# Performance work log

Measured on AMD Instinct MI355X. Metric: run time of the kernel, lower is better.

## Reference

```python
import jax, jax.numpy as jnp
import numpy as np

B, S, D, A = 4, 4096, 1024, 1024

def setup_inputs() -> dict:
    key = jax.random.key(0)
    k1, k2, k3, k4 = jax.random.split(key, 4)
    # weights scaled like keras 'random_normal' init (stddev=0.05)
    return {
        "inputs": jax.random.normal(k1, (B, S, D), dtype=jnp.float32),
        "W_q": jax.random.normal(k2, (D, A), dtype=jnp.float32) * 0.05,
        "W_k": jax.random.normal(k3, (D, A), dtype=jnp.float32) * 0.05,
        "W_v": jax.random.normal(k4, (D, A), dtype=jnp.float32) * 0.05,
    }

def reference(inputs, W_q, W_k, W_v):
    Q = jnp.einsum('bsd,da->bsa', inputs, W_q)
    K = jnp.einsum('bsd,da->bsa', inputs, W_k)
    V = jnp.einsum('bsd,da->bsa', inputs, W_v)
    # NOTE: original layer applies NO 1/sqrt(d) scaling
    scores = jnp.einsum('bqa,bka->bqk', Q, K)            # [B, S, S]
    weights = jax.nn.softmax(scores, axis=-1)
    return jnp.einsum('bqk,bka->bqa', weights, V)        # [B, S, A]
```

## Files before the change

### kernel.cpp

```cpp
#include <hip/hip_runtime.h>
#include <math.h>

constexpr int CS = 4096;
constexpr int CD = 1024;
constexpr int CA = 1024;
constexpr int CB_ = 4;

typedef unsigned short u16;
typedef __bf16 bf16x8 __attribute__((ext_vector_type(8)));
typedef float f32x4 __attribute__((ext_vector_type(4)));
typedef unsigned short u16x4 __attribute__((ext_vector_type(4)));

__device__ __forceinline__ u16 f32_to_bf16(float f) {
  unsigned u = __float_as_uint(f);
  u = (u + 0x7FFF + ((u >> 16) & 1)) >> 16;
  return (u16)u;
}
__device__ __forceinline__ float bf16_to_f32(u16 h) {
  return __uint_as_float(((unsigned)h) << 16);
}

__device__ __forceinline__ void async16(const u16* g, u16* lds_uniform) {
  __builtin_amdgcn_global_load_lds(
      (const __attribute__((address_space(1))) void*)g,
      (__attribute__((address_space(3))) void*)lds_uniform, 16, 0, 0);
}

#define ST_A256(BUF, AP, HALF)                                       \
  do {                                                               \
    const u16* _p = (AP) + roA + ((HALF) ? 128L * lda : 0L);         \
    u16* _d = &lds[(BUF)*32768 + (2 + (HALF)) * 8192 + si0 * 512];   \
    async16(_p, _d);                                                 \
    async16(_p + 32, _d + 512);                                      \
  } while (0)
#define ST_B256(BUF, BP, HALF)                                       \
  do {                                                               \
    const u16* _p = (BP) + roB + ((HALF) ? 128L * ldb : 0L);         \
    u16* _d = &lds[(BUF)*32768 + (HALF)*8192 + si0 * 512];           \
    async16(_p, _d);                                                 \
    async16(_p + 32, _d + 512);                                      \
  } while (0)

#define KITER256(T, DO_S1, DO_S2, VMW)                                        \
  do {                                                                        \
    const int buf = (T)&1;                                                    \
    const int bo_a = buf * 32768 + (2 + wr) * 8192;                           \
    const int bo_b = buf * 32768 + (wc >> 1) * 8192;                          \
    bf16x8 Bf[4][2], Am[2][2], A47[4][2];                                     \
                     \
    _Pragma("unroll") for (int n = 0; n < 4; ++n) _Pragma("unroll")           \
        for (int kk = 0; kk < 2; ++kk) Bf[n][kk] =                            \
        *(const bf16x8*)&lds[bo_b + ((nbase + n) * 2 + kk) * 512 + foff];     \
    _Pragma("unroll") for (int m = 0; m < 2; ++m) _Pragma("unroll")           \
        for (int kk = 0; kk < 2; ++kk) Am[m][kk] =                            \
        *(const bf16x8*)&lds[bo_a + (m * 2 + kk) * 512 + foff];               \
    if (DO_S1) ST_A256(buf ^ 1, a1p, 1);                                      \
    __builtin_amdgcn_s_barrier();                                             \
    asm volatile("s_waitcnt lgkmcnt(0)" ::: "memory");                        \
    __builtin_amdgcn_s_setprio(1);                                            \
    _Pragma("unroll") for (int m = 0; m < 2; ++m) _Pragma("unroll")           \
        for (int n = 0; n < 4; ++n) _Pragma("unroll")                         \
        for (int kk = 0; kk < 2; ++kk) acc[m][n] =                            \
        __builtin_amdgcn_mfma_f32_16x16x32_bf16(Am[m][kk], Bf[n][kk],         \
                                                acc[m][n], 0, 0, 0);          \
    __builtin_amdgcn_s_setprio(0);                                            \
    __builtin_amdgcn_s_barrier();                                             \
                             \
    _Pragma("unroll") for (int m = 0; m < 2; ++m) _Pragma("unroll")           \
        for (int kk = 0; kk < 2; ++kk) Am[m][kk] =                            \
        *(const bf16x8*)&lds[bo_a + ((2 + m) * 2 + kk) * 512 + foff];         \
    if (DO_S2) ST_B256(buf, b2p, 0);                                          \
    __builtin_amdgcn_s_barrier();                                             \
    asm volatile("s_waitcnt lgkmcnt(0)" ::: "memory");                        \
    __builtin_amdgcn_s_setprio(1);                                            \
    _Pragma("unroll") for (int m = 0; m < 2; ++m) _Pragma("unroll")           \
        for (int n = 0; n < 4; ++n) _Pragma("unroll")                         \
        for (int kk = 0; kk < 2; ++kk) acc[2 + m][n] =                        \
        __builtin_amdgcn_mfma_f32_16x16x32_bf16(Am[m][kk], Bf[n][kk],         \
                                                acc[2 + m][n], 0, 0, 0);      \
    __builtin_amdgcn_s_setprio(0);                                            \
    __builtin_amdgcn_s_barrier();                                             \
                             \
    _Pragma("unroll") for (int m = 0; m < 4; ++m) _Pragma("unroll")           \
        for (int kk = 0; kk < 2; ++kk) A47[m][kk] =                           \
        *(const bf16x8*)&lds[bo_a + ((4 + m) * 2 + kk) * 512 + foff];         \
    if (DO_S2) ST_B256(buf, b2p, 1);                                          \
    __builtin_amdgcn_s_barrier();                                             \
    asm volatile("s_waitcnt lgkmcnt(0)" ::: "memory");                        \
    __builtin_amdgcn_s_setprio(1);                                            \
    _Pragma("unroll") for (int m = 0; m < 2; ++m) _Pragma("unroll")           \
        for (int n = 0; n < 4; ++n) _Pragma("unroll")                         \
        for (int kk = 0; kk < 2; ++kk) acc[4 + m][n] =                        \
        __builtin_amdgcn_mfma_f32_16x16x32_bf16(A47[m][kk], Bf[n][kk],        \
                                                acc[4 + m][n], 0, 0, 0);      \
    __builtin_amdgcn_s_setprio(0);                                            \
    __builtin_amdgcn_s_barrier();                                             \
           \
    if (DO_S2) ST_A256(buf, a2p, 0);                                          \
    __builtin_amdgcn_s_barrier();                                             \
    asm volatile("s_waitcnt lgkmcnt(0)" ::: "memory");                        \
    __builtin_amdgcn_s_setprio(1);                                            \
    _Pragma("unroll") for (int m = 0; m < 2; ++m) _Pragma("unroll")           \
        for (int n = 0; n < 4; ++n) _Pragma("unroll")                         \
        for (int kk = 0; kk < 2; ++kk) acc[6 + m][n] =                        \
        __builtin_amdgcn_mfma_f32_16x16x32_bf16(A47[2 + m][kk], Bf[n][kk],    \
                                                acc[6 + m][n], 0, 0, 0);      \
    __builtin_amdgcn_s_setprio(0);                                            \
    VMW;                                                                      \
    __builtin_amdgcn_s_barrier();                                             \
  } while (0)

template <int NSEG>
__global__ __launch_bounds__(512, 2) void gemm256_nt(
    const u16* __restrict__ A0s, const u16* __restrict__ A1s,
    const u16* __restrict__ A2s, const u16* __restrict__ B0s,
    const u16* __restrict__ B1s, const u16* __restrict__ B2s,
    float* __restrict__ C, int Kd, int lda, int ldb, int ldc) {
  __shared__ u16 lds[65536];
  const int tid = threadIdx.x;
  const int wave = tid >> 6, lane = tid & 63;
  const int wr = wave >> 2, wc = wave & 3;
  const int l16 = lane & 15, quad = lane >> 4;
  const int m0 = blockIdx.y * 256, n0 = blockIdx.x * 256;
  const int foff = (l16 * 32 + quad * 8) ^ ((l16 & 8) << 1);
  const int si0 = wave * 2;
  const int srow = lane >> 2;
  const int scol = ((lane & 3) * 8) ^ ((lane & 32) ? 16 : 0);
  const long roA = (long)(m0 + wave * 16 + srow) * lda + scol;
  const long roB = (long)(n0 + wave * 16 + srow) * ldb + scol;
  const int nbase = (wc & 1) * 4;

  f32x4 acc[8][4];
#pragma unroll
  for (int i = 0; i < 8; ++i)
#pragma unroll
    for (int j = 0; j < 4; ++j) acc[i][j] = (f32x4){0.f, 0.f, 0.f, 0.f};

  const int ktps = Kd >> 6;
  const int NT = NSEG * ktps;

  int s1 = 0, k1 = 64;
  if (k1 == Kd) { k1 = 0; s1 = 1; }
  const u16* a1p = (s1 == 0 ? A0s : A1s) + k1;
  const u16* b1p = (s1 == 0 ? B0s : B1s) + k1;
  ST_B256(0, B0s, 0);
  ST_B256(0, B0s, 1);
  ST_A256(0, A0s, 0);
  ST_A256(0, A0s, 1);
  ST_B256(1, b1p, 0);
  ST_B256(1, b1p, 1);
  ST_A256(1, a1p, 0);
  (void)b1p;
  int s2 = s1, k2 = k1 + 64;
  if (k2 == Kd) { k2 = 0; ++s2; }
  const u16* a2p = (s2 == 0 ? A0s : (s2 == 1 ? A1s : A2s)) + k2;
  const u16* b2p = (s2 == 0 ? B0s : (s2 == 1 ? B1s : B2s)) + k2;
  asm volatile("s_waitcnt vmcnt(6)" ::: "memory");
  __builtin_amdgcn_s_barrier();

  for (int t = 0; t + 2 < NT; ++t) {
    KITER256(t, 1, 1, asm volatile("s_waitcnt vmcnt(6)" ::: "memory"));
    a1p = a2p;
    k2 += 64;
    if (k2 == Kd) {
      k2 = 0;
      ++s2;
      a2p = (s2 == 1 ? A1s : A2s);
      b2p = (s2 == 1 ? B1s : B2s);
    } else {
      a2p += 64;
      b2p += 64;
    }
  }
  KITER256(NT - 2, 1, 0, asm volatile("s_waitcnt vmcnt(0)" ::: "memory"));
  KITER256(NT - 1, 0, 0, ((void)0));

  const int rb0 = m0 + wr * 128 + quad * 4;
  const int cc0 = n0 + wc * 64 + l16;
#pragma unroll
  for (int m = 0; m < 8; ++m)
#pragma unroll
    for (int n = 0; n < 4; ++n) {
      const long rb = rb0 + m * 16;
      const int c = cc0 + n * 16;
#pragma unroll
      for (int r = 0; r < 4; ++r) C[(rb + r) * (long)ldc + c] = acc[m][n][r];
    }
}

__global__ __launch_bounds__(512, 2) void gemm256_qk(
    const u16* __restrict__ Xhi, const u16* __restrict__ Xlo,
    const u16* __restrict__ Whi, const u16* __restrict__ Wlo,
    u16* __restrict__ Qhi, u16* __restrict__ Qlo, u16* __restrict__ Khi,
    u16* __restrict__ Klo) {
  __shared__ u16 lds[65536];
  const int tid = threadIdx.x;
  const int wave = tid >> 6, lane = tid & 63;
  const int wr = wave >> 2, wc = wave & 3;
  const int l16 = lane & 15, quad = lane >> 4;
  const int m0 = blockIdx.y * 256, n0 = blockIdx.x * 256;
  const int region = n0 >> 10;
  const int lda = CD, ldb = CD;
  const int foff = (l16 * 32 + quad * 8) ^ ((l16 & 8) << 1);
  const int si0 = wave * 2;
  const int srow = lane >> 2;
  const int scol = ((lane & 3) * 8) ^ ((lane & 32) ? 16 : 0);
  const long roA = (long)(m0 + wave * 16 + srow) * lda + scol;
  const long roB = (long)(n0 + wave * 16 + srow) * ldb + scol;
  const int nbase = (wc & 1) * 4;

  f32x4 acc[8][4];
#pragma unroll
  for (int i = 0; i < 8; ++i)
#pragma unroll
    for (int j = 0; j < 4; ++j) acc[i][j] = (f32x4){0.f, 0.f, 0.f, 0.f};

  const u16* Asegs[3] = {Xhi, Xlo, Xhi};
  const u16* Bsegs[3] = {Whi, Whi, Wlo};
  const int NT = 48;

  const u16* a1p = Xhi + 64;
  int s2 = 0, k2 = 128;
  const u16* a2p = Xhi + 128;
  const u16* b2p = Whi + 128;
  ST_B256(0, Whi, 0);
  ST_B256(0, Whi, 1);
  ST_A256(0, Xhi, 0);
  ST_A256(0, Xhi, 1);
  ST_B256(1, Whi + 64, 0);
  ST_B256(1, Whi + 64, 1);
  ST_A256(1, Xhi + 64, 0);
  asm volatile("s_waitcnt vmcnt(6)" ::: "memory");
  __builtin_amdgcn_s_barrier();

  for (int t = 0; t + 2 < NT; ++t) {
    KITER256(t, 1, 1, asm volatile("s_waitcnt vmcnt(6)" ::: "memory"));
    a1p = a2p;
    k2 += 64;
    if (k2 == CD) {
      k2 = 0;
      ++s2;
      if (s2 < 3) {
        a2p = Asegs[s2];
        b2p = Bsegs[s2];
      }
    } else {
      a2p += 64;
      b2p += 64;
    }
  }
  KITER256(NT - 2, 1, 0, asm volatile("s_waitcnt vmcnt(0)" ::: "memory"));
  KITER256(NT - 1, 0, 0, ((void)0));

  const int rb0 = m0 + wr * 128 + quad * 4;
  const int ccl = (n0 & 1023) + wc * 64 + l16;
  u16* Chi = region ? Khi : Qhi;
  u16* Clo = region ? Klo : Qlo;
#pragma unroll
  for (int m = 0; m < 8; ++m)
#pragma unroll
    for (int n = 0; n < 4; ++n) {
      const long rb = rb0 + m * 16;
      const int c = ccl + n * 16;
#pragma unroll
      for (int r = 0; r < 4; ++r) {
        const float v = acc[m][n][r];
        const u16 h = f32_to_bf16(v);
        Chi[(rb + r) * (long)CA + c] = h;
        Clo[(rb + r) * (long)CA + c] = f32_to_bf16(v - bf16_to_f32(h));
      }
    }
}

__global__ __launch_bounds__(512, 2) void gemm256_v(
    const u16* __restrict__ Xhi, const u16* __restrict__ Wvhi,
    u16* __restrict__ Vt) {
  __shared__ u16 lds[65536];
  const int tid = threadIdx.x;
  const int wave = tid >> 6, lane = tid & 63;
  const int wr = wave >> 2, wc = wave & 3;
  const int l16 = lane & 15, quad = lane >> 4;
  const int m0 = blockIdx.y * 256, n0 = blockIdx.x * 256;
  const int lda = CD, ldb = CD;
  const int foff = (l16 * 32 + quad * 8) ^ ((l16 & 8) << 1);
  const int si0 = wave * 2;
  const int srow = lane >> 2;
  const int scol = ((lane & 3) * 8) ^ ((lane & 32) ? 16 : 0);
  const long roA = (long)(m0 + wave * 16 + srow) * lda + scol;
  const long roB = (long)(n0 + wave * 16 + srow) * ldb + scol;
  const int nbase = (wc & 1) * 4;

  f32x4 acc[8][4];
#pragma unroll
  for (int i = 0; i < 8; ++i)
#pragma unroll
    for (int j = 0; j < 4; ++j) acc[i][j] = (f32x4){0.f, 0.f, 0.f, 0.f};

  const int NT = 16;
  const u16* a1p = Xhi + 64;
  const u16* a2p = Xhi + 128;
  const u16* b2p = Wvhi + 128;
  ST_B256(0, Wvhi, 0);
  ST_B256(0, Wvhi, 1);
  ST_A256(0, Xhi, 0);
  ST_A256(0, Xhi, 1);
  ST_B256(1, Wvhi + 64, 0);
  ST_B256(1, Wvhi + 64, 1);
  ST_A256(1, Xhi + 64, 0);
  asm volatile("s_waitcnt vmcnt(6)" ::: "memory");
  __builtin_amdgcn_s_barrier();

  for (int t = 0; t + 2 < NT; ++t) {
    KITER256(t, 1, 1, asm volatile("s_waitcnt vmcnt(6)" ::: "memory"));
    a1p = a2p;
    a2p += 64;
    b2p += 64;
  }
  KITER256(NT - 2, 1, 0, asm volatile("s_waitcnt vmcnt(0)" ::: "memory"));
  KITER256(NT - 1, 0, 0, ((void)0));

  const int rb0 = m0 + wr * 128 + quad * 4;
  const int ccl = n0 + wc * 64 + l16;
#pragma unroll
  for (int m = 0; m < 8; ++m) {
    const int rg = rb0 + m * 16;
    const long vb = (long)(rg >> 12) * CA * CS;
    const int s = rg & 4095;
#pragma unroll
    for (int n = 0; n < 4; ++n) {
      const int c = ccl + n * 16;
      u16x4 p;
#pragma unroll
      for (int r = 0; r < 4; ++r) p[r] = f32_to_bf16(acc[m][n][r]);
      *(u16x4*)&Vt[vb + (long)c * CS + s] = p;
    }
  }
}

__global__ __launch_bounds__(512, 2) void gemm256_pv(
    const u16* __restrict__ P, const u16* __restrict__ Vtb,
    float* __restrict__ Cp) {
  __shared__ u16 lds[65536];
  const int tid = threadIdx.x;
  const int wave = tid >> 6, lane = tid & 63;
  const int wr = wave >> 2, wc = wave & 3;
  const int l16 = lane & 15, quad = lane >> 4;
  const int m0 = blockIdx.y * 256, n0 = blockIdx.x * 256;
  const int z = blockIdx.z;
  const int lda = CS, ldb = CS;
  const int foff = (l16 * 32 + quad * 8) ^ ((l16 & 8) << 1);
  const int si0 = wave * 2;
  const int srow = lane >> 2;
  const int scol = ((lane & 3) * 8) ^ ((lane & 32) ? 16 : 0);
  const long roA = (long)(m0 + wave * 16 + srow) * lda + scol;
  const long roB = (long)(n0 + wave * 16 + srow) * ldb + scol;
  const int nbase = (wc & 1) * 4;

  f32x4 acc[8][4];
#pragma unroll
  for (int i = 0; i < 8; ++i)
#pragma unroll
    for (int j = 0; j < 4; ++j) acc[i][j] = (f32x4){0.f, 0.f, 0.f, 0.f};

  const u16* A0 = P + (long)z * 1024;
  const u16* B0 = Vtb + (long)z * 1024;
  const int NT = 16;
  const u16* a1p = A0 + 64;
  const u16* a2p = A0 + 128;
  const u16* b2p = B0 + 128;
  ST_B256(0, B0, 0);
  ST_B256(0, B0, 1);
  ST_A256(0, A0, 0);
  ST_A256(0, A0, 1);
  ST_B256(1, B0 + 64, 0);
  ST_B256(1, B0 + 64, 1);
  ST_A256(1, A0 + 64, 0);
  asm volatile("s_waitcnt vmcnt(6)" ::: "memory");
  __builtin_amdgcn_s_barrier();

  for (int t = 0; t + 2 < NT; ++t) {
    KITER256(t, 1, 1, asm volatile("s_waitcnt vmcnt(6)" ::: "memory"));
    a1p = a2p;
    a2p += 64;
    b2p += 64;
  }
  KITER256(NT - 2, 1, 0, asm volatile("s_waitcnt vmcnt(0)" ::: "memory"));
  KITER256(NT - 1, 0, 0, ((void)0));

  float* C = Cp + (long)z * CS * CA;
  const int rb0 = m0 + wr * 128 + quad * 4;
  const int cc0 = n0 + wc * 64 + l16;
#pragma unroll
  for (int m = 0; m < 8; ++m)
#pragma unroll
    for (int n = 0; n < 4; ++n) {
      const long rb = rb0 + m * 16;
      const int c = cc0 + n * 16;
#pragma unroll
      for (int r = 0; r < 4; ++r) C[(rb + r) * (long)CA + c] = acc[m][n][r];
    }
}

#undef KITER256
#undef ST_A256
#undef ST_B256

template <int KD>
__global__ __launch_bounds__(256) void gemm_pv(const u16* __restrict__ P,
                                               const u16* __restrict__ Vtb,
                                               float* __restrict__ Cp) {
  __shared__ u16 As[128 * 32];
  __shared__ u16 Bs[128 * 32];
  const int tid = threadIdx.x;
  const int wave = tid >> 6, lane = tid & 63;
  const int quad = lane >> 4, l16 = lane & 15;
  const int m0 = blockIdx.y * 128, n0 = blockIdx.x * 128;
  const int z = blockIdx.z;
  const int wm = (wave >> 1) * 64, wn = (wave & 1) * 64;
  const int srow = lane >> 2;
  const int scol = (lane & 3) * 8;
  const int c0 = wave, c1 = wave + 4;

  const u16* Ab = P + (long)m0 * CS + (long)z * KD;
  const u16* Bb = Vtb + (long)n0 * CS + (long)z * KD;
  float* C = Cp + (long)z * CS * CA;

  f32x4 acc[4][4];
#pragma unroll
  for (int i = 0; i < 4; ++i)
#pragma unroll
    for (int j = 0; j < 4; ++j) acc[i][j] = (f32x4){0.f, 0.f, 0.f, 0.f};

  for (int k0 = 0; k0 < KD; k0 += 32) {
    async16(Ab + (long)(c0 * 16 + srow) * CS + k0 + scol, As + c0 * 512);
    async16(Ab + (long)(c1 * 16 + srow) * CS + k0 + scol, As + c1 * 512);
    async16(Bb + (long)(c0 * 16 + srow) * CS + k0 + scol, Bs + c0 * 512);
    async16(Bb + (long)(c1 * 16 + srow) * CS + k0 + scol, Bs + c1 * 512);
    __syncthreads();
    bf16x8 af[4], bfr[4];
#pragma unroll
    for (int i = 0; i < 4; ++i)
      af[i] = *(const bf16x8*)&As[(wm + i * 16 + l16) * 32 + quad * 8];
#pragma unroll
    for (int j = 0; j < 4; ++j)
      bfr[j] = *(const bf16x8*)&Bs[(wn + j * 16 + l16) * 32 + quad * 8];
#pragma unroll
    for (int i = 0; i < 4; ++i)
#pragma unroll
      for (int j = 0; j < 4; ++j)
        acc[i][j] = __builtin_amdgcn_mfma_f32_16x16x32_bf16(af[i], bfr[j],
                                                            acc[i][j], 0, 0, 0);
    __syncthreads();
  }

#pragma unroll
  for (int i = 0; i < 4; ++i) {
    const int rb = m0 + wm + i * 16 + quad * 4;
#pragma unroll
    for (int j = 0; j < 4; ++j) {
      const int c = n0 + wn + j * 16 + l16;
#pragma unroll
      for (int r = 0; r < 4; ++r) C[(long)(rb + r) * CA + c] = acc[i][j][r];
    }
  }
}

__global__ __launch_bounds__(256) void add4_f32(const float* __restrict__ p,
                                                float* __restrict__ o, int n4) {
  const int idx = blockIdx.x * 256 + threadIdx.x;
  if (idx >= n4) return;
  const long st = (long)CS * CA / 4;
  const float4 a = ((const float4*)p)[idx];
  const float4 b = ((const float4*)p)[idx + st];
  const float4 c = ((const float4*)p)[idx + 2 * st];
  const float4 d = ((const float4*)p)[idx + 3 * st];
  float4 r;
  r.x = (a.x + b.x) + (c.x + d.x);
  r.y = (a.y + b.y) + (c.y + d.y);
  r.z = (a.z + b.z) + (c.z + d.z);
  r.w = (a.w + b.w) + (c.w + d.w);
  ((float4*)o)[idx] = r;
}

__global__ __launch_bounds__(256) void wtrans_split(const float* __restrict__ W,
                                                    u16* __restrict__ Thi,
                                                    u16* __restrict__ Tlo) {
  __shared__ float t[32][33];
  const int tx = threadIdx.x & 31, ty = threadIdx.x >> 5;
  const int a0 = blockIdx.x * 32;
  const int d0 = blockIdx.y * 32;
#pragma unroll
  for (int i = 0; i < 32; i += 8)
    t[ty + i][tx] = W[(long)(d0 + ty + i) * CA + a0 + tx];
  __syncthreads();
#pragma unroll
  for (int i = 0; i < 32; i += 8) {
    const float v = t[tx][ty + i];
    const int a = a0 + ty + i, d = d0 + tx;
    const u16 h = f32_to_bf16(v);
    Thi[(long)a * CD + d] = h;
    if (Tlo) Tlo[(long)a * CD + d] = f32_to_bf16(v - bf16_to_f32(h));
  }
}

__global__ __launch_bounds__(256) void split_f32(const float* __restrict__ X,
                                                 u16* __restrict__ hi,
                                                 u16* __restrict__ lo, int n4) {
  const int idx = blockIdx.x * 256 + threadIdx.x;
  if (idx >= n4) return;
  const float4 v = ((const float4*)X)[idx];
  u16x4 h, l;
  const float vv[4] = {v.x, v.y, v.z, v.w};
#pragma unroll
  for (int i = 0; i < 4; ++i) {
    h[i] = f32_to_bf16(vv[i]);
    l[i] = f32_to_bf16(vv[i] - bf16_to_f32(h[i]));
  }
  ((u16x4*)hi)[idx] = h;
  ((u16x4*)lo)[idx] = l;
}

__global__ __launch_bounds__(256) void softmax_bf16(const float* __restrict__ Sc,
                                                    u16* __restrict__ P) {
  const long row = blockIdx.x;
  const float* p = Sc + row * 4096L;
  u16* q = P + row * 4096L;
  const int tid = threadIdx.x;

  float r[16];
#pragma unroll
  for (int i = 0; i < 16; ++i) r[i] = p[tid + (i << 8)];

  float m = r[0];
#pragma unroll
  for (int i = 1; i < 16; ++i) m = fmaxf(m, r[i]);
#pragma unroll
  for (int off = 32; off > 0; off >>= 1) m = fmaxf(m, __shfl_down(m, off));

  __shared__ float smax[4];
  __shared__ float ssum[4];
  const int lane = tid & 63;
  const int wv = tid >> 6;
  if (lane == 0) smax[wv] = m;
  __syncthreads();
  m = fmaxf(fmaxf(smax[0], smax[1]), fmaxf(smax[2], smax[3]));

  float s = 0.f;
#pragma unroll
  for (int i = 0; i < 16; ++i) {
    r[i] = __expf(r[i] - m);
    s += r[i];
  }
#pragma unroll
  for (int off = 32; off > 0; off >>= 1) s += __shfl_down(s, off);
  if (lane == 0) ssum[wv] = s;
  __syncthreads();
  s = (ssum[0] + ssum[1]) + (ssum[2] + ssum[3]);

  const float inv = 1.0f / s;
#pragma unroll
  for (int i = 0; i < 16; ++i) q[tid + (i << 8)] = f32_to_bf16(r[i] * inv);
}

extern "C" void kernel_launch(void* const* d_in, const int* in_sizes, int n_in,
                              void* d_out, int out_size, void* d_ws,
                              size_t ws_size, hipStream_t stream) {
  const float* X = (const float*)d_in[0];
  const float* Wq = (const float*)d_in[1];
  const float* Wk = (const float*)d_in[2];
  const float* Wv = (const float*)d_in[3];
  float* out = (float*)d_out;

  const size_t MB = 1 << 20;
  char* w = (char*)d_ws;
  u16* Whi = (u16*)(w + 0 * MB);
  u16* Wlo = (u16*)(w + 6 * MB);

  int nb = 1;
  if (ws_size >= 266 * MB) nb = 4;
  else if (ws_size >= 186 * MB) nb = 2;
  const bool big = ws_size >= 146 * MB;
  if (!big) nb = 1;

  const size_t bs = (size_t)CS * CA * 2;
  u16* Qhi = (u16*)(w + 10 * MB);
  u16* Qlo = (u16*)((char*)Qhi + (size_t)nb * bs);
  u16* Khi = (u16*)((char*)Qhi + (size_t)2 * nb * bs);
  u16* Klo = (u16*)((char*)Qhi + (size_t)3 * nb * bs);
  u16* Vt = (u16*)((char*)Qhi + (size_t)4 * nb * bs);
  u16* P = (u16*)((char*)Qhi + (size_t)5 * nb * bs);
  char* scb = (char*)P + 32 * MB;
  float* Sc = (float*)scb;
  u16* Xhi = (u16*)scb;
  u16* Xlo = Xhi + (size_t)nb * CS * CD;
  float* part = Sc;

  long slabQ = 4096;
  if (!big) {
    slabQ = 512;
    const size_t base = 82 * MB;
    for (long s = 4096; s >= 512; s >>= 1) {
      size_t region = (size_t)s * CS * 4;
      if (region < 16 * MB) region = 16 * MB;
      if (base + region <= ws_size) {
        slabQ = s;
        break;
      }
    }
  }

  const dim3 blk(256);

  wtrans_split<<<dim3(32, 32), blk, 0, stream>>>(Wq, Whi, Wlo);
  wtrans_split<<<dim3(32, 32), blk, 0, stream>>>(Wk, Whi + 1024 * 1024,
                                                 Wlo + 1024 * 1024);
  wtrans_split<<<dim3(32, 32), blk, 0, stream>>>(Wv, Whi + 2 * 1024 * 1024,
                                                 nullptr);

  for (int g = 0; g < CB_; g += nb) {
    split_f32<<<dim3(nb * CS * CD / 4 / 256), blk, 0, stream>>>(
        X + (long)g * CS * CD, Xhi, Xlo, nb * CS * CD / 4);

    gemm256_qk<<<dim3(8, 16 * nb), dim3(512), 0, stream>>>(
        Xhi, Xlo, Whi, Wlo, Qhi, Qlo, Khi, Klo);
    gemm256_v<<<dim3(4, 16 * nb), dim3(512), 0, stream>>>(
        Xhi, Whi + 2 * 1024 * 1024, Vt);

    for (int bb = 0; bb < nb; ++bb) {
      const int b = g + bb;
      float* outb = out + (long)b * CS * CA;
      const long qo = (long)bb * CS * CA;
      u16* Vtb = Vt + (long)bb * CA * CS;

      for (long q0 = 0; q0 < CS; q0 += slabQ) {
        const dim3 gs(CS / 256, (unsigned)(slabQ / 256));
        gemm256_nt<3><<<gs, dim3(512), 0, stream>>>(
            Qhi + qo + q0 * CA, Qlo + qo + q0 * CA, Qhi + qo + q0 * CA,
            Khi + qo, Khi + qo, Klo + qo, Sc, CA, CA, CA, CS);
        softmax_bf16<<<dim3((unsigned)slabQ), blk, 0, stream>>>(Sc,
                                                                P + q0 * CS);
      }

      if (big) {
        gemm256_pv<<<dim3(4, 16, 4), dim3(512), 0, stream>>>(P, Vtb, part);
        add4_f32<<<dim3(CS * CA / 4 / 256), blk, 0, stream>>>(part, outb,
                                                              CS * CA / 4);
      } else {
        gemm_pv<4096><<<dim3(8, 32, 1), blk, 0, stream>>>(P, Vtb, outb);
      }
    }
  }
}
```

Measured before the change: 982.0 us.

## Add XCD-aware block swizzle, batched two-way split-K PV, vectorized softmax

Adds an XCD-aware remapping of workgroup indices in all 256-tile GEMMs, so blocks sharing operand tiles land on the same L2/XCD. When the workspace allows two batches, P for both batches is kept and a single batched PV GEMM with 2-way split-K runs, followed by a 2-input add, instead of per-batch 4-way split-K with add4. Softmax now reads and writes with float4/u16x4 vector accesses. These changes target cache locality, launch count and partial-sum traffic, at the cost of more workspace and extra index arithmetic.

```diff
diff --git a/kernel.cpp b/kernel.cpp
--- a/kernel.cpp
+++ b/kernel.cpp
@@ -24,6 +24,16 @@
   __builtin_amdgcn_global_load_lds(
       (const __attribute__((address_space(1))) void*)g,
       (__attribute__((address_space(3))) void*)lds_uniform, 16, 0, 0);
+}
+
+__device__ __forceinline__ void xcd_swz(int cw, int ch, int& bx, int& by) {
+  if (cw == 0) return;
+  const int GX = gridDim.x;
+  const int lin = bx + GX * by;
+  const int xcd = lin & 7, j = lin >> 3;
+  const int ncx = GX / cw;
+  bx = (xcd % ncx) * cw + (j % cw);
+  by = (xcd / ncx) * ch + (j / cw);
 }
 
 #define ST_A256(BUF, AP, HALF)                                       \
@@ -115,13 +125,16 @@
     const u16* __restrict__ A0s, const u16* __restrict__ A1s,
     const u16* __restrict__ A2s, const u16* __restrict__ B0s,
     const u16* __restrict__ B1s, const u16* __restrict__ B2s,
-    float* __restrict__ C, int Kd, int lda, int ldb, int ldc) {
+    float* __restrict__ C, int Kd, int lda, int ldb, int ldc, int cw,
+    int ch) {
   __shared__ u16 lds[65536];
   const int tid = threadIdx.x;
   const int wave = tid >> 6, lane = tid & 63;
   const int wr = wave >> 2, wc = wave & 3;
   const int l16 = lane & 15, quad = lane >> 4;
-  const int m0 = blockIdx.y * 256, n0 = blockIdx.x * 256;
+  int bx = blockIdx.x, by = blockIdx.y;
+  xcd_swz(cw, ch, bx, by);
+  const int m0 = by * 256, n0 = bx * 256;
   const int foff = (l16 * 32 + quad * 8) ^ ((l16 & 8) << 1);
   const int si0 = wave * 2;
   const int srow = lane >> 2;
@@ -192,13 +205,15 @@
     const u16* __restrict__ Xhi, const u16* __restrict__ Xlo,
     const u16* __restrict__ Whi, const u16* __restrict__ Wlo,
     u16* __restrict__ Qhi, u16* __restrict__ Qlo, u16* __restrict__ Khi,
-    u16* __restrict__ Klo) {
+    u16* __restrict__ Klo, int cw, int ch) {
   __shared__ u16 lds[65536];
   const int tid = threadIdx.x;
   const int wave = tid >> 6, lane = tid & 63;
   const int wr = wave >> 2, wc = wave & 3;
   const int l16 = lane & 15, quad = lane >> 4;
-  const int m0 = blockIdx.y * 256, n0 = blockIdx.x * 256;
+  int bx = blockIdx.x, by = blockIdx.y;
+  xcd_swz(cw, ch, bx, by);
+  const int m0 = by * 256, n0 = bx * 256;
   const int region = n0 >> 10;
   const int lda = CD, ldb = CD;
   const int foff = (l16 * 32 + quad * 8) ^ ((l16 & 8) << 1);
@@ -274,13 +289,15 @@
 
 __global__ __launch_bounds__(512, 2) void gemm256_v(
     const u16* __restrict__ Xhi, const u16* __restrict__ Wvhi,
-    u16* __restrict__ Vt) {
+    u16* __restrict__ Vt, int cw, int ch) {
   __shared__ u16 lds[65536];
   const int tid = threadIdx.x;
   const int wave = tid >> 6, lane = tid & 63;
   const int wr = wave >> 2, wc = wave & 3;
   const int l16 = lane & 15, quad = lane >> 4;
-  const int m0 = blockIdx.y * 256, n0 = blockIdx.x * 256;
+  int bx = blockIdx.x, by = blockIdx.y;
+  xcd_swz(cw, ch, bx, by);
+  const int m0 = by * 256, n0 = bx * 256;
   const int lda = CD, ldb = CD;
   const int foff = (l16 * 32 + quad * 8) ^ ((l16 & 8) << 1);
   const int si0 = wave * 2;
@@ -339,13 +356,15 @@
 
 __global__ __launch_bounds__(512, 2) void gemm256_pv(
     const u16* __restrict__ P, const u16* __restrict__ Vtb,
-    float* __restrict__ Cp) {
+    float* __restrict__ Cp, int cw, int ch) {
   __shared__ u16 lds[65536];
   const int tid = threadIdx.x;
   const int wave = tid >> 6, lane = tid & 63;
   const int wr = wave >> 2, wc = wave & 3;
   const int l16 = lane & 15, quad = lane >> 4;
-  const int m0 = blockIdx.y * 256, n0 = blockIdx.x * 256;
+  int bx = blockIdx.x, by = blockIdx.y;
+  xcd_swz(cw, ch, bx, by);
+  const int m0 = by * 256, n0 = bx * 256;
   const int z = blockIdx.z;
   const int lda = CS, ldb = CS;
   const int foff = (l16 * 32 + quad * 8) ^ ((l16 & 8) << 1);
@@ -401,6 +420,73 @@
     }
 }
 
+__global__ __launch_bounds__(512, 2) void gemm256_pv2(
+    const u16* __restrict__ P2, const u16* __restrict__ Vt,
+    float* __restrict__ Cp, int cw, int ch) {
+  __shared__ u16 lds[65536];
+  const int tid = threadIdx.x;
+  const int wave = tid >> 6, lane = tid & 63;
+  const int wr = wave >> 2, wc = wave & 3;
+  const int l16 = lane & 15, quad = lane >> 4;
+  int bx = blockIdx.x, by = blockIdx.y;
+  xcd_swz(cw, ch, bx, by);
+  const int z = blockIdx.z;
+  const int batch = by >> 4;
+  const int m0 = (by & 15) * 256, n0 = bx * 256;
+  const int lda = CS, ldb = CS;
+  const int foff = (l16 * 32 + quad * 8) ^ ((l16 & 8) << 1);
+  const int si0 = wave * 2;
+  const int srow = lane >> 2;
+  const int scol = ((lane & 3) * 8) ^ ((lane & 32) ? 16 : 0);
+  const long roA = (long)(m0 + wave * 16 + srow) * lda + scol;
+  const long roB = (long)(n0 + wave * 16 + srow) * ldb + scol;
+  const int nbase = (wc & 1) * 4;
+
+  f32x4 acc[8][4];
+#pragma unroll
+  for (int i = 0; i < 8; ++i)
+#pragma unroll
+    for (int j = 0; j < 4; ++j) acc[i][j] = (f32x4){0.f, 0.f, 0.f, 0.f};
+
+  const u16* A0 = P2 + (long)batch * CS * CS + (long)z * 2048;
+  const u16* B0 = Vt + (long)batch * CA * CS + (long)z * 2048;
+  const int NT = 32;
+  const u16* a1p = A0 + 64;
+  const u16* a2p = A0 + 128;
+  const u16* b2p = B0 + 128;
+  ST_B256(0, B0, 0);
+  ST_B256(0, B0, 1);
+  ST_A256(0, A0, 0);
+  ST_A256(0, A0, 1);
+  ST_B256(1, B0 + 64, 0);
+  ST_B256(1, B0 + 64, 1);
+  ST_A256(1, A0 + 64, 0);
+  asm volatile("s_waitcnt vmcnt(6)" ::: "memory");
+  __builtin_amdgcn_s_barrier();
+
+  for (int t = 0; t + 2 < NT; ++t) {
+    KITER256(t, 1, 1, asm volatile("s_waitcnt vmcnt(6)" ::: "memory"));
+    a1p = a2p;
+    a2p += 64;
+    b2p += 64;
+  }
+  KITER256(NT - 2, 1, 0, asm volatile("s_waitcnt vmcnt(0)" ::: "memory"));
+  KITER256(NT - 1, 0, 0, ((void)0));
+
+  float* C = Cp + ((long)batch * 2 + z) * CS * CA;
+  const int rb0 = m0 + wr * 128 + quad * 4;
+  const int cc0 = n0 + wc * 64 + l16;
+#pragma unroll
+  for (int m = 0; m < 8; ++m)
+#pragma unroll
+    for (int n = 0; n < 4; ++n) {
+      const long rb = rb0 + m * 16;
+      const int c = cc0 + n * 16;
+#pragma unroll
+      for (int r = 0; r < 4; ++r) C[(rb + r) * (long)CA + c] = acc[m][n][r];
+    }
+}
+
 #undef KITER256
 #undef ST_A256
 #undef ST_B256
@@ -482,6 +568,21 @@
   ((float4*)o)[idx] = r;
 }
 
+__global__ __launch_bounds__(256) void add2_f32(const float* __restrict__ a,
+                                                const float* __restrict__ b,
+                                                float* __restrict__ o, int n4) {
+  const int idx = blockIdx.x * 256 + threadIdx.x;
+  if (idx >= n4) return;
+  const float4 x = ((const float4*)a)[idx];
+  const float4 y = ((const float4*)b)[idx];
+  float4 r;
+  r.x = x.x + y.x;
+  r.y = x.y + y.y;
+  r.z = x.z + y.z;
+  r.w = x.w + y.w;
+  ((float4*)o)[idx] = r;
+}
+
 __global__ __launch_bounds__(256) void wtrans_split(const float* __restrict__ W,
                                                     u16* __restrict__ Thi,
                                                     u16* __restrict__ Tlo) {
@@ -523,13 +624,21 @@
 __global__ __launch_bounds__(256) void softmax_bf16(const float* __restrict__ Sc,
                                                     u16* __restrict__ P) {
   const long row = blockIdx.x;
-  const float* p = Sc + row * 4096L;
-  u16* q = P + row * 4096L;
+  const float4* p4 = (const float4*)(Sc + row * 4096L);
+  u16x4* q4 = (u16x4*)(P + row * 4096L);
   const int tid = threadIdx.x;
 
+  float4 v[4];
+#pragma unroll
+  for (int i = 0; i < 4; ++i) v[i] = p4[tid + (i << 8)];
   float r[16];
 #pragma unroll
-  for (int i = 0; i < 16; ++i) r[i] = p[tid + (i << 8)];
+  for (int i = 0; i < 4; ++i) {
+    r[4 * i] = v[i].x;
+    r[4 * i + 1] = v[i].y;
+    r[4 * i + 2] = v[i].z;
+    r[4 * i + 3] = v[i].w;
+  }
 
   float m = r[0];
 #pragma unroll
@@ -559,7 +668,12 @@
 
   const float inv = 1.0f / s;
 #pragma unroll
-  for (int i = 0; i < 16; ++i) q[tid + (i << 8)] = f32_to_bf16(r[i] * inv);
+  for (int i = 0; i < 4; ++i) {
+    u16x4 h;
+#pragma unroll
+    for (int k = 0; k < 4; ++k) h[k] = f32_to_bf16(r[4 * i + k] * inv);
+    q4[tid + (i << 8)] = h;
+  }
 }
 
 extern "C" void kernel_launch(void* const* d_in, const int* in_sizes, int n_in,
@@ -581,6 +695,7 @@
   else if (ws_size >= 186 * MB) nb = 2;
   const bool big = ws_size >= 146 * MB;
   if (!big) nb = 1;
+  const bool bigP = (nb == 2) && (ws_size >= 218 * MB);
 
   const size_t bs = (size_t)CS * CA * 2;
   u16* Qhi = (u16*)(w + 10 * MB);
@@ -589,7 +704,7 @@
   u16* Klo = (u16*)((char*)Qhi + (size_t)3 * nb * bs);
   u16* Vt = (u16*)((char*)Qhi + (size_t)4 * nb * bs);
   u16* P = (u16*)((char*)Qhi + (size_t)5 * nb * bs);
-  char* scb = (char*)P + 32 * MB;
+  char* scb = (char*)P + (bigP ? 64 : 32) * MB;
   float* Sc = (float*)scb;
   u16* Xhi = (u16*)scb;
   u16* Xlo = Xhi + (size_t)nb * CS * CD;
@@ -609,6 +724,17 @@
     }
   }
 
+  auto pick = [](int gx, int gy, int& cw, int& ch) {
+    cw = 0;
+    ch = 0;
+    const int nwg = gx * gy;
+    if ((nwg & 31) || (gx & 3)) return;
+    const int h = nwg >> 5;
+    if (h == 0 || (gy % h)) return;
+    cw = 4;
+    ch = h;
+  };
+
   const dim3 blk(256);
 
   wtrans_split<<<dim3(32, 32), blk, 0, stream>>>(Wq, Whi, Wlo);
@@ -617,37 +743,59 @@
   wtrans_split<<<dim3(32, 32), blk, 0, stream>>>(Wv, Whi + 2 * 1024 * 1024,
                                                  nullptr);
 
+  int cwqk, chqk, cwv, chv, cws, chs, cwp, chp, cwp2, chp2;
+  pick(8, 16 * nb, cwqk, chqk);
+  pick(4, 16 * nb, cwv, chv);
+  pick(16, (int)(slabQ / 256) == 0 ? 1 : (int)(slabQ / 256), cws, chs);
+  if (slabQ < 256) { cws = 0; chs = 0; }
+  pick(4, 16, cwp, chp);
+  pick(4, 32, cwp2, chp2);
+
   for (int g = 0; g < CB_; g += nb) {
     split_f32<<<dim3(nb * CS * CD / 4 / 256), blk, 0, stream>>>(
         X + (long)g * CS * CD, Xhi, Xlo, nb * CS * CD / 4);
 
     gemm256_qk<<<dim3(8, 16 * nb), dim3(512), 0, stream>>>(
-        Xhi, Xlo, Whi, Wlo, Qhi, Qlo, Khi, Klo);
+        Xhi, Xlo, Whi, Wlo, Qhi, Qlo, Khi, Klo, cwqk, chqk);
     gemm256_v<<<dim3(4, 16 * nb), dim3(512), 0, stream>>>(
-        Xhi, Whi + 2 * 1024 * 1024, Vt);
+        Xhi, Whi + 2 * 1024 * 1024, Vt, cwv, chv);
 
     for (int bb = 0; bb < nb; ++bb) {
-      const int b = g + bb;
-      float* outb = out + (long)b * CS * CA;
-      const long qo = (long)bb * CS * CA;
-      u16* Vtb = Vt + (long)bb * CA * CS;
+      u16* Pb = P + (bigP ? (long)bb * CS * CS : 0);
 
       for (long q0 = 0; q0 < CS; q0 += slabQ) {
+        const long qo = (long)bb * CS * CA;
         const dim3 gs(CS / 256, (unsigned)(slabQ / 256));
         gemm256_nt<3><<<gs, dim3(512), 0, stream>>>(
             Qhi + qo + q0 * CA, Qlo + qo + q0 * CA, Qhi + qo + q0 * CA,
-            Khi + qo, Khi + qo, Klo + qo, Sc, CA, CA, CA, CS);
+            Khi + qo, Khi + qo, Klo + qo, Sc, CA, CA, CA, CS, cws, chs);
         softmax_bf16<<<dim3((unsigned)slabQ), blk, 0, stream>>>(Sc,
-                                                                P + q0 * CS);
+                                                                Pb + q0 * CS);
       }
-
-      if (big) {
-        gemm256_pv<<<dim3(4, 16, 4), dim3(512), 0, stream>>>(P, Vtb, part);
-        add4_f32<<<dim3(CS * CA / 4 / 256), blk, 0, stream>>>(part, outb,
-                                                              CS * CA / 4);
-      } else {
-        gemm_pv<4096><<<dim3(8, 32, 1), blk, 0, stream>>>(P, Vtb, outb);
+    }
+
+    if (bigP) {
+      gemm256_pv2<<<dim3(4, 32, 2), dim3(512), 0, stream>>>(P, Vt, part,
+                                                            cwp2, chp2);
+      for (int bb = 0; bb < nb; ++bb) {
+        const long pl = (long)CS * CA;
+        add2_f32<<<dim3(CS * CA / 4 / 256), blk, 0, stream>>>(
+            part + (long)bb * 2 * pl, part + ((long)bb * 2 + 1) * pl,
+            out + (long)(g + bb) * pl, CS * CA / 4);
       }
-    }
-  }
-}
+    } else {
+      for (int bb = 0; bb < nb; ++bb) {
+        float* outb = out + (long)(g + bb) * CS * CA;
+        u16* Vtb = Vt + (long)bb * CA * CS;
+        if (big) {
+          gemm256_pv<<<dim3(4, 16, 4), dim3(512), 0, stream>>>(P, Vtb, part,
+                                                               cwp, chp);
+          add4_f32<<<dim3(CS * CA / 4 / 256), blk, 0, stream>>>(part, outb,
+                                                                CS * CA / 4);
+        } else {
+          gemm_pv<4096><<<dim3(8, 32, 1), blk, 0, stream>>>(P, Vtb, outb);
+        }
+      }
+    }
+  }
+}
```

Result: faster. 951.2 us (-3.1%).
